# Performance work log

Hardware: AMD Instinct MI355X
Metric: run time of the kernel (lower is better)

Reference implementation:

```python
import jax, jax.numpy as jnp
import numpy as np

N, K, D_IN, D_OUT = 50000, 16, 128, 256
C1, C2 = D_OUT // 4, D_OUT // 2  # 64, 128
E = N * K


def _lin(key, din, dout):
    return jax.random.normal(key, (din, dout), jnp.float32) * 0.02


def setup_inputs() -> dict:
    key = jax.random.key(0)
    ks = jax.random.split(key, 16)
    x = jax.random.normal(ks[0], (N, D_IN), jnp.float32)
    pos = jax.random.normal(ks[1], (N, 3), jnp.float32)
    normals = jax.random.normal(ks[2], (N, 3), jnp.float32)
    batch = jnp.zeros((N,), jnp.int32)
    # fixed k-regular graph standing in for knn_graph(pos, K); src != dst so
    # darboux's sqrt(|pos_j-pos_i|^2) is smooth everywhere
    dst = jnp.repeat(jnp.arange(N, dtype=jnp.int32), K)            # [E]
    off = jax.random.randint(ks[3], (E,), 1, N, jnp.int32)
    src = (dst + off) % N                                          # [E]
    edge_index = jnp.stack([src, dst])                             # [2,E]
    inp = dict(x=x, pos=pos, batch=batch, normals=normals, edge_index=edge_index)

    def add_mlp(name, k, din, dout):
        inp[name + '_w'] = _lin(k, din, dout)
        inp[name + '_b'] = jnp.zeros((dout,), jnp.float32)
        inp[name + '_g'] = jnp.ones((dout,), jnp.float32)
        inp[name + '_bt'] = jnp.zeros((dout,), jnp.float32)

    add_mlp('mlp1', ks[4], D_IN, D_OUT // 8)
    add_mlp('sc', ks[5], D_IN, D_OUT)
    add_mlp('mlp2', ks[6], C2, D_OUT)
    add_mlp('enc1', ks[7], 8, C1 // 2)
    inp['att1_w'] = _lin(ks[8], C1, C1)
    add_mlp('post1', ks[9], C1, C1)
    add_mlp('enc2', ks[10], 8, C2 // 2)
    inp['att2_w'] = _lin(ks[11], C2, C2)
    add_mlp('post2', ks[12], C2, C2)
    return inp


def _bn(h, g, bt, eps=1e-6):
    # BatchNorm1d, training-mode batch statistics (biased variance)
    m = h.mean(0)
    v = jnp.mean((h - m) ** 2, axis=0)
    return (h - m) * jax.lax.rsqrt(v + eps) * g + bt


def _lrelu(h):
    return jnp.where(h >= 0, h, 0.2 * h)


def _smlp(h, w, b, g, bt, act=True):
    # SharedMLP layer: Linear -> BN(eps=1e-6) -> LeakyReLU(0.2) (act optional)
    h = _bn(h @ w + b, g, bt)
    return _lrelu(h) if act else h


def _darboux(pi, pj, ni, nj):
    eps = 1e-10
    d = pj - pi                                            # [E,3]
    dot = lambda a, b: jnp.sum(a * b, axis=1, keepdims=True)
    nrm = lambda a: jnp.sqrt(jnp.sum(a * a, axis=1, keepdims=True))
    dist = nrm(d)
    lni, lnj = nrm(ni), nrm(nj)
    uq = jnp.cross(d, ni); vq = jnp.cross(uq, ni)
    uk = jnp.cross(d, nj); vk = jnp.cross(uk, nj)
    luq, lvq, luk, lvk = nrm(uq), nrm(vq), nrm(uk), nrm(vk)
    return jnp.concatenate([
        dist,
        dot(d, ni) / (dist * lni + eps),
        dot(d, nj) / (dist * lnj + eps),
        dot(ni, nj) / (lni * lnj + eps),
        dot(uq, uk) / (luq * luk + eps),
        dot(vq, vk) / (lvq * lvk + eps),
        dot(uq, vk) / (luq * lvk + eps),
        dot(vq, uk) / (lvq * luk + eps),
    ], axis=1)                                             # [E,8]


def _seg_softmax(h, idx, n):
    m = jax.ops.segment_max(h, idx, num_segments=n)        # [N,C]
    e = jnp.exp(h - m[idx])
    s = jax.ops.segment_sum(e, idx, num_segments=n)
    return e / (s[idx] + 1e-16)


def _lfa(src, dst, n, x, pos, normals, ew, eb, eg, ebt, aw, pw, pb, pg, pbt):
    rel = _darboux(pos[dst], pos[src], normals[dst], normals[src])  # [E,8]
    lse = _smlp(rel, ew, eb, eg, ebt)                               # [E,C/2]
    lf = jnp.concatenate([x[src], lse], axis=1)                     # [E,C]
    att = lf @ aw                                                   # [E,C]
    scores = _seg_softmax(att, dst, n)
    agg = jax.ops.segment_sum(scores * lf, dst, num_segments=n)     # [N,C]
    return _smlp(agg, pw, pb, pg, pbt)


def reference(x, pos, batch, normals, edge_index,
              mlp1_w, mlp1_b, mlp1_g, mlp1_bt,
              sc_w, sc_b, sc_g, sc_bt,
              mlp2_w, mlp2_b, mlp2_g, mlp2_bt,
              enc1_w, enc1_b, enc1_g, enc1_bt, att1_w,
              post1_w, post1_b, post1_g, post1_bt,
              enc2_w, enc2_b, enc2_g, enc2_bt, att2_w,
              post2_w, post2_b, post2_g, post2_bt):
    n = x.shape[0]
    src, dst = edge_index[0], edge_index[1]
    shortcut = _smlp(x, sc_w, sc_b, sc_g, sc_bt, act=False)         # [N,d_out]
    h = _smlp(x, mlp1_w, mlp1_b, mlp1_g, mlp1_bt)                   # [N,d_out//8]
    h = _lfa(src, dst, n, h, pos, normals,
             enc1_w, enc1_b, enc1_g, enc1_bt, att1_w,
             post1_w, post1_b, post1_g, post1_bt)                   # [N,d_out//4]
    h = _lfa(src, dst, n, h, pos, normals,
             enc2_w, enc2_b, enc2_g, enc2_bt, att2_w,
             post2_w, post2_b, post2_g, post2_bt)                   # [N,d_out//2]
    h = _smlp(h, mlp2_w, mlp2_b, mlp2_g, mlp2_bt, act=False)        # [N,d_out]
    return _lrelu(h + shortcut)
```

## Files before the change

### kernel.cpp

```cpp
#include <hip/hip_runtime.h>
#include <hip/hip_bf16.h>
#include <math.h>


typedef __attribute__((ext_vector_type(8))) short short8;
typedef __attribute__((ext_vector_type(4))) float floatx4;

#define NPART 16
#define PSTRIDE 4096

__device__ __forceinline__ float lrelu_f(float v) { return v >= 0.f ? v : 0.2f * v; }

__device__ __forceinline__ uint asu(float f) {
    union { float f; uint u; } c; c.f = f; return c.u;
}
__device__ __forceinline__ unsigned short f2bf(float f) {
    union { __hip_bfloat16 h; unsigned short u; } cv;
    cv.h = __float2bfloat16(f);
    return cv.u;
}
__device__ __forceinline__ unsigned short f2bf_r(float f) {
    return (unsigned short)((asu(f) + 0x8000u) >> 16);
}
__device__ __forceinline__ uint pack2bf_r(float lo, float hi) {
    return ((asu(lo) + 0x8000u) >> 16) | ((asu(hi) + 0x8000u) & 0xFFFF0000u);
}
__device__ __forceinline__ float bf2f(unsigned short u) {
    union { unsigned short u; __hip_bfloat16 h; } cv;
    cv.u = u;
    return __bfloat162float(cv.h);
}

struct PrepSeg { const float* src; short* dst; int cnt; int Cout; int KK; };
struct PrepArgs { PrepSeg seg[6]; };

__global__ void wprep_kernel(PrepArgs pa)
{
    int gid = blockIdx.x * 256 + threadIdx.x;
    int base = 0;
    for (int s = 0; s < 6; s++) {
        int c = pa.seg[s].cnt;
        if (gid < base + c) {
            int fi = gid - base;
            const float* w = pa.seg[s].src;
            const int Cout = pa.seg[s].Cout, KK = pa.seg[s].KK;
            const int l15 = fi & 15, g = (fi >> 4) & 3, rest = fi >> 6;
            const int kk = rest % KK, nt = rest / KK;
            const int col = nt * 16 + l15;
            short8 v;
#pragma unroll
            for (int e = 0; e < 8; e++)
                v[e] = (short)f2bf(w[(size_t)(kk * 32 + g * 8 + e) * Cout + col]);
            *reinterpret_cast<short8*>(pa.seg[s].dst + (size_t)fi * 8) = v;
            return;
        }
        base += c;
    }
}

template<int DIN, int DOUT, int TM>
__global__ void lin_stats_kernel(const float* __restrict__ in, const float* __restrict__ w,
                                 const float* __restrict__ b, float* __restrict__ out,
                                 double* __restrict__ st, int n)
{
    constexpr int CT = DOUT;
    constexpr int RG = 256 / CT;
    constexpr int ROWS = TM * RG;
    __shared__ float xtile[ROWS][DIN];
    double* stp = st + (blockIdx.x & (NPART - 1)) * PSTRIDE;
    const int row0 = blockIdx.x * ROWS;
    for (int idx = threadIdx.x; idx < ROWS * DIN; idx += 256) {
        int r = idx / DIN, j = idx - r * DIN;
        int rr = row0 + r;
        xtile[r][j] = (rr < n) ? in[(size_t)rr * DIN + j] : 0.f;
    }
    __syncthreads();
    const int c  = threadIdx.x % CT;
    const int rg = threadIdx.x / CT;
    float acc[TM];
    const float bv = b[c];
#pragma unroll
    for (int t = 0; t < TM; t++) acc[t] = bv;
    for (int j = 0; j < DIN; j++) {
        float wv = w[(size_t)j * DOUT + c];
#pragma unroll
        for (int t = 0; t < TM; t++) acc[t] = fmaf(xtile[rg * TM + t][j], wv, acc[t]);
    }
    float s = 0.f, s2 = 0.f;
#pragma unroll
    for (int t = 0; t < TM; t++) {
        int rr = row0 + rg * TM + t;
        if (rr < n) {
            out[(size_t)rr * DOUT + c] = acc[t];
            s += acc[t];
            s2 = fmaf(acc[t], acc[t], s2);
        }
    }
    __syncthreads();
    float* ls  = &xtile[0][0];
    float* ls2 = ls + 256;
    ls[threadIdx.x] = s; ls2[threadIdx.x] = s2;
    __syncthreads();
    if (rg == 0) {
#pragma unroll
        for (int g = 1; g < RG; g++) { s += ls[g * CT + c]; s2 += ls2[g * CT + c]; }
        atomicAdd(&stp[c], (double)s);
        atomicAdd(&stp[DOUT + c], (double)s2);
    }
}

template<bool AFF, bool IN16>
__global__ __launch_bounds__(256)
void lin_mfma_kernel(const void* __restrict__ inv, const float* __restrict__ aff,
                     const short* __restrict__ wp, const float* __restrict__ b,
                     unsigned short* __restrict__ out16, double* __restrict__ st, int n)
{
    __shared__ __align__(16) char aS[64 * 256];
    const int tid = threadIdx.x;
    const int w = tid >> 6, grp = (tid >> 4) & 3, l15 = tid & 15, lane = tid & 63;
    const int row0 = blockIdx.x * 64;
    double* stp = st + (blockIdx.x & (NPART - 1)) * PSTRIDE;
    {
        const int r = tid >> 2;
        const int p = tid & 3;
        const int chbase = p * 32;
        const int gr = row0 + r;
        if (gr < n) {
#pragma unroll
            for (int u = 0; u < 4; u++) {
                float h[8];
                if constexpr (IN16) {
                    const unsigned short* hrow = (const unsigned short*)inv + (size_t)gr * 128 + chbase + u * 8;
                    uint4 raw = *reinterpret_cast<const uint4*>(hrow);
                    h[0] = bf2f((unsigned short)(raw.x & 0xFFFF)); h[1] = bf2f((unsigned short)(raw.x >> 16));
                    h[2] = bf2f((unsigned short)(raw.y & 0xFFFF)); h[3] = bf2f((unsigned short)(raw.y >> 16));
                    h[4] = bf2f((unsigned short)(raw.z & 0xFFFF)); h[5] = bf2f((unsigned short)(raw.z >> 16));
                    h[6] = bf2f((unsigned short)(raw.w & 0xFFFF)); h[7] = bf2f((unsigned short)(raw.w >> 16));
                } else {
                    const float* hrow = (const float*)inv + (size_t)gr * 128 + chbase + u * 8;
                    float4 h0 = *reinterpret_cast<const float4*>(hrow);
                    float4 h1 = *reinterpret_cast<const float4*>(hrow + 4);
                    h[0] = h0.x; h[1] = h0.y; h[2] = h0.z; h[3] = h0.w;
                    h[4] = h1.x; h[5] = h1.y; h[6] = h1.z; h[7] = h1.w;
                }
                if constexpr (AFF) {
                    const float* ar = aff + chbase + u * 8;
                    const float* cr = aff + 128 + chbase + u * 8;
#pragma unroll
                    for (int i2 = 0; i2 < 8; i2++)
                        h[i2] = lrelu_f(fmaf(h[i2], ar[i2], cr[i2]));
                }
                uint4 pk;
                pk.x = pack2bf_r(h[0], h[1]); pk.y = pack2bf_r(h[2], h[3]);
                pk.z = pack2bf_r(h[4], h[5]); pk.w = pack2bf_r(h[6], h[7]);
                const int unit = (chbase >> 3) + u;
                *reinterpret_cast<uint4*>(aS + r * 256 + ((unit ^ (r & 7)) << 4)) = pk;
            }
        }
    }
    __syncthreads();

    short8 B[4][4]; float bias[4];
#pragma unroll
    for (int t = 0; t < 4; t++) {
        const int nt = w * 4 + t;
        bias[t] = b[nt * 16 + l15];
#pragma unroll
        for (int kk = 0; kk < 4; kk++)
            B[t][kk] = *reinterpret_cast<const short8*>(wp + (size_t)(((nt * 4 + kk) * 4 + grp) * 16 + l15) * 8);
    }
    float ssum[4] = {0.f, 0.f, 0.f, 0.f}, ssq[4] = {0.f, 0.f, 0.f, 0.f};
#pragma unroll
    for (int mt = 0; mt < 4; mt++) {
        short8 a[4];
        const int arow = mt * 16 + l15;
#pragma unroll
        for (int kk = 0; kk < 4; kk++)
            a[kk] = *reinterpret_cast<const short8*>(aS + arow * 256 + ((((kk << 2) + grp) ^ (arow & 7)) << 4));
#pragma unroll
        for (int t = 0; t < 4; t++) {
            floatx4 acc = {bias[t], bias[t], bias[t], bias[t]};
#pragma unroll
            for (int kk = 0; kk < 4; kk++)
                acc = __builtin_amdgcn_mfma_f32_16x16x32_bf16(a[kk], B[t][kk], acc, 0, 0, 0);
            const int c = (w * 4 + t) * 16 + l15;
#pragma unroll
            for (int r = 0; r < 4; r++) {
                const int grow = row0 + mt * 16 + grp * 4 + r;
                if (grow < n) {
                    out16[(size_t)grow * 256 + c] = f2bf_r(acc[r]);
                    ssum[t] += acc[r];
                    ssq[t] = fmaf(acc[r], acc[r], ssq[t]);
                }
            }
        }
    }
#pragma unroll
    for (int t = 0; t < 4; t++) {
        float s = ssum[t], q = ssq[t];
        s += __shfl_xor(s, 16); s += __shfl_xor(s, 32);
        q += __shfl_xor(q, 16); q += __shfl_xor(q, 32);
        if (lane < 16) {
            const int c = (w * 4 + t) * 16 + l15;
            atomicAdd(&stp[c], (double)s);
            atomicAdd(&stp[256 + c], (double)q);
        }
    }
}

__global__ __launch_bounds__(256)
void edge_enc_kernel(const int* __restrict__ src, const float* __restrict__ pos,
                     const float* __restrict__ nrm, unsigned short* __restrict__ rel16,
                     int E, double* __restrict__ stM)
{
    float s8[8] = {0, 0, 0, 0, 0, 0, 0, 0};
    float M[36];
#pragma unroll
    for (int k = 0; k < 36; k++) M[k] = 0.f;
    const int tid = threadIdx.x;

    for (int e = blockIdx.x * 256 + tid; e < E; e += gridDim.x * 256) {
        const int d = e >> 4;
        const int s = src[e];
        const float pix = pos[3 * d], piy = pos[3 * d + 1], piz = pos[3 * d + 2];
        const float pjx = pos[3 * s], pjy = pos[3 * s + 1], pjz = pos[3 * s + 2];
        const float nix = nrm[3 * d], niy = nrm[3 * d + 1], niz = nrm[3 * d + 2];
        const float njx = nrm[3 * s], njy = nrm[3 * s + 1], njz = nrm[3 * s + 2];
        const float dx = pjx - pix, dy = pjy - piy, dz = pjz - piz;
        const float dist = sqrtf(dx * dx + dy * dy + dz * dz);
        const float lni = sqrtf(nix * nix + niy * niy + niz * niz);
        const float lnj = sqrtf(njx * njx + njy * njy + njz * njz);
        const float uqx = dy * niz - dz * niy, uqy = dz * nix - dx * niz, uqz = dx * niy - dy * nix;
        const float vqx = uqy * niz - uqz * niy, vqy = uqz * nix - uqx * niz, vqz = uqx * niy - uqy * nix;
        const float ukx = dy * njz - dz * njy, uky = dz * njx - dx * njz, ukz = dx * njy - dy * njx;
        const float vkx = uky * njz - ukz * njy, vky = ukz * njx - ukx * njz, vkz = ukx * njy - uky * njx;
        const float luq = sqrtf(uqx * uqx + uqy * uqy + uqz * uqz);
        const float lvq = sqrtf(vqx * vqx + vqy * vqy + vqz * vqz);
        const float luk = sqrtf(ukx * ukx + uky * uky + ukz * ukz);
        const float lvk = sqrtf(vkx * vkx + vky * vky + vkz * vkz);
        const float eps = 1e-10f;
        float rv[8];
        rv[0] = dist;
        rv[1] = (dx * nix + dy * niy + dz * niz) / (dist * lni + eps);
        rv[2] = (dx * njx + dy * njy + dz * njz) / (dist * lnj + eps);
        rv[3] = (nix * njx + niy * njy + niz * njz) / (lni * lnj + eps);
        rv[4] = (uqx * ukx + uqy * uky + uqz * ukz) / (luq * luk + eps);
        rv[5] = (vqx * vkx + vqy * vky + vqz * vkz) / (lvq * lvk + eps);
        rv[6] = (uqx * vkx + uqy * vky + uqz * vkz) / (luq * lvk + eps);
        rv[7] = (vqx * ukx + vqy * uky + vqz * ukz) / (lvq * luk + eps);
        uint4 pk;
        pk.x = pack2bf_r(rv[0], rv[1]); pk.y = pack2bf_r(rv[2], rv[3]);
        pk.z = pack2bf_r(rv[4], rv[5]); pk.w = pack2bf_r(rv[6], rv[7]);
        *reinterpret_cast<uint4*>(rel16 + (size_t)e * 8) = pk;
#pragma unroll
        for (int i = 0; i < 8; i++) s8[i] += rv[i];
#pragma unroll
        for (int i = 0; i < 8; i++)
#pragma unroll
            for (int j = i; j < 8; j++)
                M[i * 8 - (i * (i - 1)) / 2 + (j - i)] = fmaf(rv[i], rv[j], M[i * 8 - (i * (i - 1)) / 2 + (j - i)]);
    }
#pragma unroll
    for (int k = 0; k < 8; k++) {
        float v = s8[k];
        v += __shfl_xor(v, 1); v += __shfl_xor(v, 2); v += __shfl_xor(v, 4);
        v += __shfl_xor(v, 8); v += __shfl_xor(v, 16); v += __shfl_xor(v, 32);
        s8[k] = v;
    }
#pragma unroll
    for (int k = 0; k < 36; k++) {
        float v = M[k];
        v += __shfl_xor(v, 1); v += __shfl_xor(v, 2); v += __shfl_xor(v, 4);
        v += __shfl_xor(v, 8); v += __shfl_xor(v, 16); v += __shfl_xor(v, 32);
        M[k] = v;
    }
    __shared__ float red[4][44];
    const int w = tid >> 6, lane = tid & 63;
    if (lane == 0) {
#pragma unroll
        for (int k = 0; k < 8; k++) red[w][k] = s8[k];
#pragma unroll
        for (int k = 0; k < 36; k++) red[w][8 + k] = M[k];
    }
    __syncthreads();
    if (tid < 44) {
        float tot = red[0][tid] + red[1][tid] + red[2][tid] + red[3][tid];
        atomicAdd(&stM[(blockIdx.x & (NPART - 1)) * PSTRIDE + tid], (double)tot);
    }
}

__global__ void enc_finalize_kernel(const double* __restrict__ stM,
    const float* __restrict__ ew1, const float* __restrict__ eb1,
    const float* __restrict__ g1, const float* __restrict__ bt1, float* __restrict__ ac1,
    const float* __restrict__ ew2, const float* __restrict__ eb2,
    const float* __restrict__ g2, const float* __restrict__ bt2, float* __restrict__ ac2,
    float Ef)
{
    __shared__ double SM[44];
    const int tid = threadIdx.x;
    if (tid < 44) {
        double a = 0;
        for (int p = 0; p < NPART; p++) a += stM[p * PSTRIDE + tid];
        SM[tid] = a;
    }
    __syncthreads();
    if (tid < 96) {
        const bool is2 = tid < 64;
        const int c = is2 ? tid : tid - 64;
        const int HCc = is2 ? 64 : 32;
        const float* ew = is2 ? ew2 : ew1;
        const float b = (is2 ? eb2 : eb1)[c];
        float wv[8];
#pragma unroll
        for (int j = 0; j < 8; j++) wv[j] = ew[j * HCc + c];
        double dot = 0.0, quad = 0.0;
#pragma unroll
        for (int i = 0; i < 8; i++) {
            dot += SM[i] * (double)wv[i];
#pragma unroll
            for (int j = i; j < 8; j++) {
                const double mij = SM[8 + i * 8 - (i * (i - 1)) / 2 + (j - i)];
                quad += mij * (double)wv[i] * (double)wv[j] * ((i == j) ? 1.0 : 2.0);
            }
        }
        const double sum   = dot + (double)Ef * b;
        const double sumsq = quad + 2.0 * b * dot + (double)Ef * b * b;
        const double m = sum / Ef;
        const double v = sumsq / Ef - m * m;
        const float rstd = (float)(1.0 / sqrt(v + 1e-6));
        const float a = rstd * (is2 ? g2 : g1)[c];
        float* ac = is2 ? ac2 : ac1;
        ac[c] = a;
        ac[HCc + c] = fmaf(-(float)m, a, (is2 ? bt2 : bt1)[c]);
    }
}

struct FinSeg { const double* st; const float* g; const float* bt; float* ac; int C; float cnt; };
struct FinArgs { FinSeg seg[3]; };

__global__ void finalize_multi_kernel(FinArgs fa)
{
    FinSeg s = fa.seg[blockIdx.x];
    int c = threadIdx.x;
    if (c < s.C) {
        double sm = 0.0, sq = 0.0;
#pragma unroll
        for (int p = 0; p < NPART; p++) {
            sm += s.st[p * PSTRIDE + c];
            sq += s.st[p * PSTRIDE + s.C + c];
        }
        double m = sm / (double)s.cnt;
        double v = sq / (double)s.cnt - m * m;
        float rstd = (float)(1.0 / sqrt(v + 1e-6));
        float a = rstd * s.g[c];
        s.ac[c] = a;
        s.ac[s.C + c] = fmaf(-(float)m, a, s.bt[c]);
    }
}

template<int C, bool IN16>
__global__ void bnconv_kernel(const void* __restrict__ hv, const float* __restrict__ ac,
                              unsigned short* __restrict__ o, size_t total8)
{
    size_t i = (size_t)blockIdx.x * blockDim.x + threadIdx.x;
    size_t stride = (size_t)gridDim.x * blockDim.x;
    for (; i < total8; i += stride) {
        const size_t b = i * 8;
        const int c = (int)(b & (size_t)(C - 1));
        float h[8];
        if constexpr (IN16) {
            uint4 raw = *reinterpret_cast<const uint4*>((const unsigned short*)hv + b);
            h[0] = bf2f((unsigned short)(raw.x & 0xFFFF)); h[1] = bf2f((unsigned short)(raw.x >> 16));
            h[2] = bf2f((unsigned short)(raw.y & 0xFFFF)); h[3] = bf2f((unsigned short)(raw.y >> 16));
            h[4] = bf2f((unsigned short)(raw.z & 0xFFFF)); h[5] = bf2f((unsigned short)(raw.z >> 16));
            h[6] = bf2f((unsigned short)(raw.w & 0xFFFF)); h[7] = bf2f((unsigned short)(raw.w >> 16));
        } else {
            float4 h0 = *reinterpret_cast<const float4*>((const float*)hv + b);
            float4 h1 = *reinterpret_cast<const float4*>((const float*)hv + b + 4);
            h[0] = h0.x; h[1] = h0.y; h[2] = h0.z; h[3] = h0.w;
            h[4] = h1.x; h[5] = h1.y; h[6] = h1.z; h[7] = h1.w;
        }
        const float* ar = ac + c;
        const float* cr = ac + C + c;
        uint4 pk;
        pk.x = pack2bf_r(lrelu_f(fmaf(h[0], ar[0], cr[0])), lrelu_f(fmaf(h[1], ar[1], cr[1])));
        pk.y = pack2bf_r(lrelu_f(fmaf(h[2], ar[2], cr[2])), lrelu_f(fmaf(h[3], ar[3], cr[3])));
        pk.z = pack2bf_r(lrelu_f(fmaf(h[4], ar[4], cr[4])), lrelu_f(fmaf(h[5], ar[5], cr[5])));
        pk.w = pack2bf_r(lrelu_f(fmaf(h[6], ar[6], cr[6])), lrelu_f(fmaf(h[7], ar[7], cr[7])));
        *reinterpret_cast<uint4*>(o + b) = pk;
    }
}

template<int C, int NODES>
__global__ __launch_bounds__(256)
void lfa11_kernel(const unsigned short* __restrict__ hbn,
                  const unsigned short* __restrict__ rel16,
                  const int* __restrict__ src,
                  const float* __restrict__ ew, const float* __restrict__ eb,
                  const float* __restrict__ encac,
                  const short* __restrict__ attp, const short* __restrict__ postp,
                  const float* __restrict__ postb,
                  unsigned short* __restrict__ out16, double* __restrict__ st, int n)
{
    constexpr int HC = C / 2, NT = C / 16, NTW = NT / 4, KK = C / 32, ROWB = 2 * C;
    constexpr int ROWS = NODES * 16;
    constexpr int TPR = 256 / ROWS;
    constexpr int NTE = HC / 16;
    constexpr int NCOMB = (NODES * NTE) / 4;
    constexpr int NSTEP = 4 / NTE;

    __shared__ __align__(16) char lfS[ROWS * ROWB];
    __shared__ __align__(16) char aggS[16 * ROWB];

    const int tid = threadIdx.x;
    const int lane = tid & 63, w = tid >> 6, grp = (tid >> 4) & 3, l15 = tid & 15;
    const int node0 = blockIdx.x * NODES;
    const int e0g = node0 * 16;
    const int Etot = n * 16;
    const int kk_sel = (w * NTW) >> 1;
    double* stp = st + (blockIdx.x & (NPART - 1)) * PSTRIDE;

    if constexpr (NODES < 16) {
        for (int i = tid; i < (16 - NODES) * ROWB / 16; i += 256)
            reinterpret_cast<uint4*>(aggS + NODES * ROWB)[i] = (uint4){0, 0, 0, 0};
    }

    short8 Batt[NTW][KK], Bsel[NTW];
#pragma unroll
    for (int t = 0; t < NTW; t++) {
        const int nt = w * NTW + t;
#pragma unroll
        for (int kk = 0; kk < KK; kk++)
            Batt[t][kk] = *reinterpret_cast<const short8*>(attp + (size_t)(((nt * KK + kk) * 4 + grp) * 16 + l15) * 8);
        const int ng = ((nt & 1) << 1) | (l15 >> 3);
#pragma unroll
        for (int e = 0; e < 8; e++)
            Bsel[t][e] = (grp == ng && (l15 & 7) == e) ? (short)0x3F80 : (short)0;
    }

    const int etile = w % NTE;
    const int cc = etile * 16 + l15;
    short8 Benc = {0, 0, 0, 0, 0, 0, 0, 0};
    if (grp == 0) {
#pragma unroll
        for (int j = 0; j < 8; j++) Benc[j] = (short)f2bf(ew[j * HC + cc]);
    }
    const float encA = encac[cc];
    const float encB2 = fmaf(encA, eb[cc], encac[HC + cc]);
    const int cfull = HC + cc;
    const int cuE = cfull >> 3, subE = (cfull & 7) * 2;

    {
        const int r = (TPR == 1) ? tid : (tid / TPR);
        const int p = (TPR == 1) ? 0 : (tid % TPR);
        constexpr int CHT = HC / TPR;
        const int chb = p * CHT;
        const int eg = e0g + r;
        if (eg < Etot) {
            const int s = src[eg];
            const unsigned short* hrow = hbn + (size_t)s * HC + chb;
#pragma unroll
            for (int u = 0; u < CHT / 8; u++) {
                uint4 pk = *reinterpret_cast<const uint4*>(hrow + u * 8);
                const int unit = (chb >> 3) + u;
                *reinterpret_cast<uint4*>(lfS + r * ROWB + ((unit ^ (r & 7)) << 4)) = pk;
            }
        }
    }

    {
        const int nodeStart = w / NTE;
#pragma unroll
        for (int j = 0; j < NCOMB; j++) {
            const int node = nodeStart + j * NSTEP;
            const int r0 = node * 16;
            int eg = e0g + r0 + l15;
            if (eg >= Etot) eg = Etot - 1;
            const short8 Arel = *reinterpret_cast<const short8*>(rel16 + (size_t)eg * 8);
            floatx4 accE = {0.f, 0.f, 0.f, 0.f};
            accE = __builtin_amdgcn_mfma_f32_16x16x32_bf16(Arel, Benc, accE, 0, 0, 0);
#pragma unroll
            for (int r = 0; r < 4; r++) {
                const int row = r0 + grp * 4 + r;
                const float tv = lrelu_f(fmaf(accE[r], encA, encB2));
                *reinterpret_cast<unsigned short*>(lfS + row * ROWB + ((cuE ^ (row & 7)) << 4) + subE) = f2bf_r(tv);
            }
        }
    }
    __syncthreads();

    for (int mt = 0; mt < NODES; ++mt) {
        const int arow = mt * 16 + l15;
        const char* rbase = lfS + arow * ROWB;
        const int x7 = l15 & 7;
        short8 a[KK];
#pragma unroll
        for (int kk = 0; kk < KK; kk++)
            a[kk] = *reinterpret_cast<const short8*>(rbase + ((((kk << 2) + grp) ^ x7) << 4));
        const short8 asel = *reinterpret_cast<const short8*>(rbase + ((((kk_sel << 2) + grp) ^ x7) << 4));
        floatx4 acc[NTW], Lc[NTW];
#pragma unroll
        for (int t = 0; t < NTW; t++) {
            acc[t] = (floatx4){0.f, 0.f, 0.f, 0.f};
            Lc[t] = (floatx4){0.f, 0.f, 0.f, 0.f};
        }
#pragma unroll
        for (int t = 0; t < NTW; t++)
            Lc[t] = __builtin_amdgcn_mfma_f32_16x16x32_bf16(asel, Bsel[t], Lc[t], 0, 0, 0);
#pragma unroll
        for (int kk = 0; kk < KK; kk++)
#pragma unroll
            for (int t = 0; t < NTW; t++)
                acc[t] = __builtin_amdgcn_mfma_f32_16x16x32_bf16(a[kk], Batt[t][kk], acc[t], 0, 0, 0);

#pragma unroll
        for (int t = 0; t < NTW; t++) {
            float e0 = __expf(acc[t][0]), e1 = __expf(acc[t][1]);
            float e2 = __expf(acc[t][2]), e3 = __expf(acc[t][3]);
            float ss = (e0 + e1) + (e2 + e3);
            ss += __shfl_xor(ss, 16);
            ss += __shfl_xor(ss, 32);
            const float inv = 1.f / (ss + 1e-16f);
            float av = fmaf(e0, Lc[t][0], fmaf(e1, Lc[t][1], fmaf(e2, Lc[t][2], e3 * Lc[t][3])));
            av += __shfl_xor(av, 16);
            av += __shfl_xor(av, 32);
            av *= inv;
            if (lane < 16) {
                const int c = (w * NTW + t) * 16 + l15;
                const int cu = c >> 3, sub = (c & 7) * 2;
                *reinterpret_cast<unsigned short*>(aggS + mt * ROWB + ((cu ^ (mt & 7)) << 4) + sub) = f2bf_r(av);
            }
        }
    }
    __syncthreads();

    short8 Bpost[NTW][KK]; float pb[NTW];
#pragma unroll
    for (int t = 0; t < NTW; t++) {
        const int nt = w * NTW + t;
        pb[t] = postb[nt * 16 + l15];
#pragma unroll
        for (int kk = 0; kk < KK; kk++)
            Bpost[t][kk] = *reinterpret_cast<const short8*>(postp + (size_t)(((nt * KK + kk) * 4 + grp) * 16 + l15) * 8);
    }
    short8 ag[KK];
#pragma unroll
    for (int kk = 0; kk < KK; kk++)
        ag[kk] = *reinterpret_cast<const short8*>(aggS + l15 * ROWB + ((((kk << 2) + grp) ^ (l15 & 7)) << 4));
    floatx4 accP[NTW];
#pragma unroll
    for (int t = 0; t < NTW; t++) accP[t] = (floatx4){0.f, 0.f, 0.f, 0.f};
#pragma unroll
    for (int kk = 0; kk < KK; kk++)
#pragma unroll
        for (int t = 0; t < NTW; t++)
            accP[t] = __builtin_amdgcn_mfma_f32_16x16x32_bf16(ag[kk], Bpost[t][kk], accP[t], 0, 0, 0);
#pragma unroll
    for (int t = 0; t < NTW; t++) {
        const int c = (w * NTW + t) * 16 + l15;
        float s = 0.f, q = 0.f;
#pragma unroll
        for (int r = 0; r < 4; r++) {
            const int nb = grp * 4 + r;
            if (nb < NODES && node0 + nb < n) {
                const float v = accP[t][r] + pb[t];
                out16[(size_t)(node0 + nb) * C + c] = f2bf_r(v);
                s += v;
                q = fmaf(v, v, q);
            }
        }
        s += __shfl_xor(s, 16); s += __shfl_xor(s, 32);
        q += __shfl_xor(q, 16); q += __shfl_xor(q, 32);
        if (lane < 16) {
            atomicAdd(&stp[c], (double)s);
            atomicAdd(&stp[C + c], (double)q);
        }
    }
}

__global__ void final_kernel(float* __restrict__ out, const unsigned short* __restrict__ m2,
                             const unsigned short* __restrict__ xs,
                             const float* __restrict__ ac2, const float* __restrict__ acs,
                             int total4)
{
    int i = blockIdx.x * 256 + threadIdx.x;
    const int stride = gridDim.x * 256;
    for (; i < total4; i += stride) {
        ushort4 mv = reinterpret_cast<const ushort4*>(m2)[i];
        ushort4 xv = reinterpret_cast<const ushort4*>(xs)[i];
        const int c = (i & 63) << 2;
        float4 a2 = *reinterpret_cast<const float4*>(ac2 + c);
        float4 b2 = *reinterpret_cast<const float4*>(ac2 + 256 + c);
        float4 as = *reinterpret_cast<const float4*>(acs + c);
        float4 bs = *reinterpret_cast<const float4*>(acs + 256 + c);
        float4 v;
        v.x = lrelu_f(fmaf(bf2f(mv.x), a2.x, b2.x) + fmaf(bf2f(xv.x), as.x, bs.x));
        v.y = lrelu_f(fmaf(bf2f(mv.y), a2.y, b2.y) + fmaf(bf2f(xv.y), as.y, bs.y));
        v.z = lrelu_f(fmaf(bf2f(mv.z), a2.z, b2.z) + fmaf(bf2f(xv.z), as.z, bs.z));
        v.w = lrelu_f(fmaf(bf2f(mv.w), a2.w, b2.w) + fmaf(bf2f(xv.w), as.w, bs.w));
        reinterpret_cast<float4*>(out)[i] = v;
    }
}

extern "C" void kernel_launch(void* const* d_in, const int* in_sizes, int n_in,
                              void* d_out, int out_size, void* d_ws, size_t ws_size,
                              hipStream_t stream)
{
    const float* x       = (const float*)d_in[0];
    const float* pos     = (const float*)d_in[1];
    const float* normals = (const float*)d_in[3];
    const int*   eidx    = (const int*)d_in[4];

    const float* mlp1_w = (const float*)d_in[5];
    const float* mlp1_b = (const float*)d_in[6];
    const float* mlp1_g = (const float*)d_in[7];
    const float* mlp1_bt= (const float*)d_in[8];
    const float* sc_w   = (const float*)d_in[9];
    const float* sc_b   = (const float*)d_in[10];
    const float* sc_g   = (const float*)d_in[11];
    const float* sc_bt  = (const float*)d_in[12];
    const float* mlp2_w = (const float*)d_in[13];
    const float* mlp2_b = (const float*)d_in[14];
    const float* mlp2_g = (const float*)d_in[15];
    const float* mlp2_bt= (const float*)d_in[16];
    const float* enc1_w = (const float*)d_in[17];
    const float* enc1_b = (const float*)d_in[18];
    const float* enc1_g = (const float*)d_in[19];
    const float* enc1_bt= (const float*)d_in[20];
    const float* att1_w = (const float*)d_in[21];
    const float* post1_w = (const float*)d_in[22];
    const float* post1_b = (const float*)d_in[23];
    const float* post1_g = (const float*)d_in[24];
    const float* post1_bt= (const float*)d_in[25];
    const float* enc2_w = (const float*)d_in[26];
    const float* enc2_b = (const float*)d_in[27];
    const float* enc2_g = (const float*)d_in[28];
    const float* enc2_bt= (const float*)d_in[29];
    const float* att2_w = (const float*)d_in[30];
    const float* post2_w = (const float*)d_in[31];
    const float* post2_b = (const float*)d_in[32];
    const float* post2_g = (const float*)d_in[33];
    const float* post2_bt= (const float*)d_in[34];

    float* out = (float*)d_out;

    const int n = in_sizes[0] / 128;
    const int E = in_sizes[4] / 2;
    const int* srcArr = eidx;

    char* base = (char*)d_ws;
    double* stats  = (double*)base;
    float*  affine = (float*)(base + 524288);
    short*  wprep  = (short*)(base + 540672);
    unsigned short* rel16 = (unsigned short*)(base + 786432);
    unsigned short* xs16  = rel16 + (size_t)E * 8;
    unsigned short* m2pre = xs16 + (size_t)n * 256;
    float*  h1   = (float*)(m2pre + (size_t)n * 256);
    unsigned short* hA16 = (unsigned short*)(h1 + (size_t)n * 32);
    unsigned short* hB16 = hA16 + (size_t)n * 64;
    unsigned short* h1bn = hB16;
    unsigned short* hAbn = (unsigned short*)h1;

    short* att1p = wprep;
    short* post1p = wprep + 4096;
    short* att2p = wprep + 8192;
    short* post2p = wprep + 24576;
    short* scp   = wprep + 40960;
    short* mlp2p = wprep + 73728;

    const int OF_MLP1 = 0, OF_ENCM = 64, OF_POST1 = 128, OF_POST2 = 512, OF_SC = 768, OF_MLP2 = 1280;
    const int AF_MLP1 = 0, AF_ENC1 = 64, AF_POST1 = 128, AF_ENC2 = 256,
              AF_POST2 = 512, AF_SC = 768, AF_MLP2 = 1280;

    hipMemsetAsync(stats, 0, NPART * 32768, stream);

    PrepArgs pa;
    pa.seg[0] = {att1_w,  att1p,  512,  64,  2};
    pa.seg[1] = {post1_w, post1p, 512,  64,  2};
    pa.seg[2] = {att2_w,  att2p,  2048, 128, 4};
    pa.seg[3] = {post2_w, post2p, 2048, 128, 4};
    pa.seg[4] = {sc_w,    scp,    4096, 256, 4};
    pa.seg[5] = {mlp2_w,  mlp2p,  4096, 256, 4};
    wprep_kernel<<<52, 256, 0, stream>>>(pa);

    lin_stats_kernel<128, 32, 8><<<(n + 63) / 64, 256, 0, stream>>>(x, mlp1_w, mlp1_b, h1, stats + OF_MLP1, n);
    lin_mfma_kernel<false, false><<<(n + 63) / 64, 256, 0, stream>>>(x, nullptr, scp, sc_b, xs16, stats + OF_SC, n);

    edge_enc_kernel<<<512, 256, 0, stream>>>(srcArr, pos, normals, rel16, E, stats + OF_ENCM);

    FinArgs f1;
    f1.seg[0] = {stats + OF_MLP1, mlp1_g, mlp1_bt, affine + AF_MLP1, 32, (float)n};
    f1.seg[1] = f1.seg[0]; f1.seg[2] = f1.seg[0];
    finalize_multi_kernel<<<1, 256, 0, stream>>>(f1);
    enc_finalize_kernel<<<1, 128, 0, stream>>>(stats + OF_ENCM,
        enc1_w, enc1_b, enc1_g, enc1_bt, affine + AF_ENC1,
        enc2_w, enc2_b, enc2_g, enc2_bt, affine + AF_ENC2, (float)E);

    bnconv_kernel<32, false><<<1024, 256, 0, stream>>>(h1, affine + AF_MLP1, h1bn, (size_t)n * 32 / 8);

    lfa11_kernel<64, 16><<<(n + 15) / 16, 256, 0, stream>>>(h1bn, rel16, srcArr, enc1_w, enc1_b,
        affine + AF_ENC1, att1p, post1p, post1_b, hA16, stats + OF_POST1, n);
    FinArgs f2;
    f2.seg[0] = {stats + OF_POST1, post1_g, post1_bt, affine + AF_POST1, 64, (float)n};
    f2.seg[1] = f2.seg[0]; f2.seg[2] = f2.seg[0];
    finalize_multi_kernel<<<1, 256, 0, stream>>>(f2);

    bnconv_kernel<64, true><<<1024, 256, 0, stream>>>(hA16, affine + AF_POST1, hAbn, (size_t)n * 64 / 8);

    lfa11_kernel<128, 8><<<(n + 7) / 8, 256, 0, stream>>>(hAbn, rel16, srcArr, enc2_w, enc2_b,
        affine + AF_ENC2, att2p, post2p, post2_b, hB16, stats + OF_POST2, n);
    FinArgs f3;
    f3.seg[0] = {stats + OF_POST2, post2_g, post2_bt, affine + AF_POST2, 128, (float)n};
    f3.seg[1] = f3.seg[0]; f3.seg[2] = f3.seg[0];
    finalize_multi_kernel<<<1, 256, 0, stream>>>(f3);

    lin_mfma_kernel<true, true><<<(n + 63) / 64, 256, 0, stream>>>(hB16, affine + AF_POST2, mlp2p, mlp2_b,
        m2pre, stats + OF_MLP2, n);
    FinArgs f4;
    f4.seg[0] = {stats + OF_MLP2, mlp2_g, mlp2_bt, affine + AF_MLP2, 256, (float)n};
    f4.seg[1] = {stats + OF_SC,   sc_g,   sc_bt,   affine + AF_SC,   256, (float)n};
    f4.seg[2] = f4.seg[0];
    finalize_multi_kernel<<<2, 256, 0, stream>>>(f4);

    final_kernel<<<2048, 256, 0, stream>>>(out, m2pre, xs16, affine + AF_MLP2, affine + AF_SC, n * 64);
}
```

Before: 258.3 us.

## Fuse mlp1 linear into shortcut MFMA kernel and process two node tiles per iteration

```diff
diff --git a/kernel.cpp b/kernel.cpp
--- a/kernel.cpp
+++ b/kernel.cpp
@@ -32,13 +32,13 @@
 }
 
 struct PrepSeg { const float* src; short* dst; int cnt; int Cout; int KK; };
-struct PrepArgs { PrepSeg seg[6]; };
+struct PrepArgs { PrepSeg seg[7]; };
 
 __global__ void wprep_kernel(PrepArgs pa)
 {
     int gid = blockIdx.x * 256 + threadIdx.x;
     int base = 0;
-    for (int s = 0; s < 6; s++) {
+    for (int s = 0; s < 7; s++) {
         int c = pa.seg[s].cnt;
         if (gid < base + c) {
             int fi = gid - base;
@@ -58,68 +58,20 @@
     }
 }
 
-template<int DIN, int DOUT, int TM>
-__global__ void lin_stats_kernel(const float* __restrict__ in, const float* __restrict__ w,
-                                 const float* __restrict__ b, float* __restrict__ out,
-                                 double* __restrict__ st, int n)
-{
-    constexpr int CT = DOUT;
-    constexpr int RG = 256 / CT;
-    constexpr int ROWS = TM * RG;
-    __shared__ float xtile[ROWS][DIN];
-    double* stp = st + (blockIdx.x & (NPART - 1)) * PSTRIDE;
-    const int row0 = blockIdx.x * ROWS;
-    for (int idx = threadIdx.x; idx < ROWS * DIN; idx += 256) {
-        int r = idx / DIN, j = idx - r * DIN;
-        int rr = row0 + r;
-        xtile[r][j] = (rr < n) ? in[(size_t)rr * DIN + j] : 0.f;
-    }
-    __syncthreads();
-    const int c  = threadIdx.x % CT;
-    const int rg = threadIdx.x / CT;
-    float acc[TM];
-    const float bv = b[c];
-#pragma unroll
-    for (int t = 0; t < TM; t++) acc[t] = bv;
-    for (int j = 0; j < DIN; j++) {
-        float wv = w[(size_t)j * DOUT + c];
-#pragma unroll
-        for (int t = 0; t < TM; t++) acc[t] = fmaf(xtile[rg * TM + t][j], wv, acc[t]);
-    }
-    float s = 0.f, s2 = 0.f;
-#pragma unroll
-    for (int t = 0; t < TM; t++) {
-        int rr = row0 + rg * TM + t;
-        if (rr < n) {
-            out[(size_t)rr * DOUT + c] = acc[t];
-            s += acc[t];
-            s2 = fmaf(acc[t], acc[t], s2);
-        }
-    }
-    __syncthreads();
-    float* ls  = &xtile[0][0];
-    float* ls2 = ls + 256;
-    ls[threadIdx.x] = s; ls2[threadIdx.x] = s2;
-    __syncthreads();
-    if (rg == 0) {
-#pragma unroll
-        for (int g = 1; g < RG; g++) { s += ls[g * CT + c]; s2 += ls2[g * CT + c]; }
-        atomicAdd(&stp[c], (double)s);
-        atomicAdd(&stp[DOUT + c], (double)s2);
-    }
-}
-
-template<bool AFF, bool IN16>
+template<bool AFF, bool IN16, bool MLP1>
 __global__ __launch_bounds__(256)
 void lin_mfma_kernel(const void* __restrict__ inv, const float* __restrict__ aff,
                      const short* __restrict__ wp, const float* __restrict__ b,
-                     unsigned short* __restrict__ out16, double* __restrict__ st, int n)
+                     unsigned short* __restrict__ out16, double* __restrict__ st,
+                     const short* __restrict__ wp1, const float* __restrict__ b1,
+                     unsigned short* __restrict__ out1, double* __restrict__ st1, int n)
 {
     __shared__ __align__(16) char aS[64 * 256];
     const int tid = threadIdx.x;
     const int w = tid >> 6, grp = (tid >> 4) & 3, l15 = tid & 15, lane = tid & 63;
     const int row0 = blockIdx.x * 64;
-    double* stp = st + (blockIdx.x & (NPART - 1)) * PSTRIDE;
+    const int poff = (blockIdx.x & (NPART - 1)) * PSTRIDE;
+    double* stp = st + poff;
     {
         const int r = tid >> 2;
         const int p = tid & 3;
@@ -204,6 +156,47 @@
             const int c = (w * 4 + t) * 16 + l15;
             atomicAdd(&stp[c], (double)s);
             atomicAdd(&stp[256 + c], (double)q);
+        }
+    }
+
+    if constexpr (MLP1) {
+        if (w < 2) {
+            double* stp1 = st1 + poff;
+            const float bias1 = b1[w * 16 + l15];
+            short8 B1[4];
+#pragma unroll
+            for (int kk = 0; kk < 4; kk++)
+                B1[kk] = *reinterpret_cast<const short8*>(wp1 + (size_t)(((w * 4 + kk) * 4 + grp) * 16 + l15) * 8);
+            float s1 = 0.f, q1 = 0.f;
+#pragma unroll
+            for (int mt = 0; mt < 4; mt++) {
+                short8 a[4];
+                const int arow = mt * 16 + l15;
+#pragma unroll
+                for (int kk = 0; kk < 4; kk++)
+                    a[kk] = *reinterpret_cast<const short8*>(aS + arow * 256 + ((((kk << 2) + grp) ^ (arow & 7)) << 4));
+                floatx4 acc = {bias1, bias1, bias1, bias1};
+#pragma unroll
+                for (int kk = 0; kk < 4; kk++)
+                    acc = __builtin_amdgcn_mfma_f32_16x16x32_bf16(a[kk], B1[kk], acc, 0, 0, 0);
+                const int c = w * 16 + l15;
+#pragma unroll
+                for (int r = 0; r < 4; r++) {
+                    const int grow = row0 + mt * 16 + grp * 4 + r;
+                    if (grow < n) {
+                        out1[(size_t)grow * 32 + c] = f2bf_r(acc[r]);
+                        s1 += acc[r];
+                        q1 = fmaf(acc[r], acc[r], q1);
+                    }
+                }
+            }
+            s1 += __shfl_xor(s1, 16); s1 += __shfl_xor(s1, 32);
+            q1 += __shfl_xor(q1, 16); q1 += __shfl_xor(q1, 32);
+            if (lane < 16) {
+                const int c = w * 16 + l15;
+                atomicAdd(&stp1[c], (double)s1);
+                atomicAdd(&stp1[32 + c], (double)q1);
+            }
         }
     }
 }
@@ -358,8 +351,8 @@
     }
 }
 
-template<int C, bool IN16>
-__global__ void bnconv_kernel(const void* __restrict__ hv, const float* __restrict__ ac,
+template<int C>
+__global__ void bnconv_kernel(const unsigned short* __restrict__ hv, const float* __restrict__ ac,
                               unsigned short* __restrict__ o, size_t total8)
 {
     size_t i = (size_t)blockIdx.x * blockDim.x + threadIdx.x;
@@ -367,19 +360,12 @@
     for (; i < total8; i += stride) {
         const size_t b = i * 8;
         const int c = (int)(b & (size_t)(C - 1));
+        uint4 raw = *reinterpret_cast<const uint4*>(hv + b);
         float h[8];
-        if constexpr (IN16) {
-            uint4 raw = *reinterpret_cast<const uint4*>((const unsigned short*)hv + b);
-            h[0] = bf2f((unsigned short)(raw.x & 0xFFFF)); h[1] = bf2f((unsigned short)(raw.x >> 16));
-            h[2] = bf2f((unsigned short)(raw.y & 0xFFFF)); h[3] = bf2f((unsigned short)(raw.y >> 16));
-            h[4] = bf2f((unsigned short)(raw.z & 0xFFFF)); h[5] = bf2f((unsigned short)(raw.z >> 16));
-            h[6] = bf2f((unsigned short)(raw.w & 0xFFFF)); h[7] = bf2f((unsigned short)(raw.w >> 16));
-        } else {
-            float4 h0 = *reinterpret_cast<const float4*>((const float*)hv + b);
-            float4 h1 = *reinterpret_cast<const float4*>((const float*)hv + b + 4);
-            h[0] = h0.x; h[1] = h0.y; h[2] = h0.z; h[3] = h0.w;
-            h[4] = h1.x; h[5] = h1.y; h[6] = h1.z; h[7] = h1.w;
-        }
+        h[0] = bf2f((unsigned short)(raw.x & 0xFFFF)); h[1] = bf2f((unsigned short)(raw.x >> 16));
+        h[2] = bf2f((unsigned short)(raw.y & 0xFFFF)); h[3] = bf2f((unsigned short)(raw.y >> 16));
+        h[4] = bf2f((unsigned short)(raw.z & 0xFFFF)); h[5] = bf2f((unsigned short)(raw.z >> 16));
+        h[6] = bf2f((unsigned short)(raw.w & 0xFFFF)); h[7] = bf2f((unsigned short)(raw.w >> 16));
         const float* ar = ac + c;
         const float* cr = ac + C + c;
         uint4 pk;
@@ -393,7 +379,7 @@
 
 template<int C, int NODES>
 __global__ __launch_bounds__(256)
-void lfa11_kernel(const unsigned short* __restrict__ hbn,
+void lfa12_kernel(const unsigned short* __restrict__ hbn,
                   const unsigned short* __restrict__ rel16,
                   const int* __restrict__ src,
                   const float* __restrict__ ew, const float* __restrict__ eb,
@@ -489,46 +475,68 @@
     }
     __syncthreads();
 
-    for (int mt = 0; mt < NODES; ++mt) {
-        const int arow = mt * 16 + l15;
-        const char* rbase = lfS + arow * ROWB;
+    for (int mt0 = 0; mt0 < NODES; mt0 += 2) {
         const int x7 = l15 & 7;
-        short8 a[KK];
+        const int arowA = mt0 * 16 + l15;
+        const int arowB = arowA + 16;
+        const char* rbA = lfS + arowA * ROWB;
+        const char* rbB = lfS + arowB * ROWB;
+        short8 aA[KK], aB[KK];
+#pragma unroll
+        for (int kk = 0; kk < KK; kk++) {
+            aA[kk] = *reinterpret_cast<const short8*>(rbA + ((((kk << 2) + grp) ^ x7) << 4));
+            aB[kk] = *reinterpret_cast<const short8*>(rbB + ((((kk << 2) + grp) ^ x7) << 4));
+        }
+        const short8 aselA = *reinterpret_cast<const short8*>(rbA + ((((kk_sel << 2) + grp) ^ x7) << 4));
+        const short8 aselB = *reinterpret_cast<const short8*>(rbB + ((((kk_sel << 2) + grp) ^ x7) << 4));
+        floatx4 accA[NTW], accB[NTW], LcA[NTW], LcB[NTW];
+#pragma unroll
+        for (int t = 0; t < NTW; t++) {
+            accA[t] = (floatx4){0.f, 0.f, 0.f, 0.f};
+            accB[t] = (floatx4){0.f, 0.f, 0.f, 0.f};
+            LcA[t] = (floatx4){0.f, 0.f, 0.f, 0.f};
+            LcB[t] = (floatx4){0.f, 0.f, 0.f, 0.f};
+        }
+#pragma unroll
+        for (int t = 0; t < NTW; t++) {
+            LcA[t] = __builtin_amdgcn_mfma_f32_16x16x32_bf16(aselA, Bsel[t], LcA[t], 0, 0, 0);
+            LcB[t] = __builtin_amdgcn_mfma_f32_16x16x32_bf16(aselB, Bsel[t], LcB[t], 0, 0, 0);
+        }
 #pragma unroll
         for (int kk = 0; kk < KK; kk++)
-            a[kk] = *reinterpret_cast<const short8*>(rbase + ((((kk << 2) + grp) ^ x7) << 4));
-        const short8 asel = *reinterpret_cast<const short8*>(rbase + ((((kk_sel << 2) + grp) ^ x7) << 4));
-        floatx4 acc[NTW], Lc[NTW];
+#pragma unroll
+            for (int t = 0; t < NTW; t++) {
+                accA[t] = __builtin_amdgcn_mfma_f32_16x16x32_bf16(aA[kk], Batt[t][kk], accA[t], 0, 0, 0);
+                accB[t] = __builtin_amdgcn_mfma_f32_16x16x32_bf16(aB[kk], Batt[t][kk], accB[t], 0, 0, 0);
+            }
+
 #pragma unroll
         for (int t = 0; t < NTW; t++) {
-            acc[t] = (floatx4){0.f, 0.f, 0.f, 0.f};
-            Lc[t] = (floatx4){0.f, 0.f, 0.f, 0.f};
-        }
-#pragma unroll
-        for (int t = 0; t < NTW; t++)
-            Lc[t] = __builtin_amdgcn_mfma_f32_16x16x32_bf16(asel, Bsel[t], Lc[t], 0, 0, 0);
-#pragma unroll
-        for (int kk = 0; kk < KK; kk++)
-#pragma unroll
-            for (int t = 0; t < NTW; t++)
-                acc[t] = __builtin_amdgcn_mfma_f32_16x16x32_bf16(a[kk], Batt[t][kk], acc[t], 0, 0, 0);
-
-#pragma unroll
-        for (int t = 0; t < NTW; t++) {
-            float e0 = __expf(acc[t][0]), e1 = __expf(acc[t][1]);
-            float e2 = __expf(acc[t][2]), e3 = __expf(acc[t][3]);
-            float ss = (e0 + e1) + (e2 + e3);
-            ss += __shfl_xor(ss, 16);
-            ss += __shfl_xor(ss, 32);
-            const float inv = 1.f / (ss + 1e-16f);
-            float av = fmaf(e0, Lc[t][0], fmaf(e1, Lc[t][1], fmaf(e2, Lc[t][2], e3 * Lc[t][3])));
-            av += __shfl_xor(av, 16);
-            av += __shfl_xor(av, 32);
-            av *= inv;
+            float e0A = __expf(accA[t][0]), e1A = __expf(accA[t][1]);
+            float e2A = __expf(accA[t][2]), e3A = __expf(accA[t][3]);
+            float e0B = __expf(accB[t][0]), e1B = __expf(accB[t][1]);
+            float e2B = __expf(accB[t][2]), e3B = __expf(accB[t][3]);
+            float ssA = (e0A + e1A) + (e2A + e3A);
+            float ssB = (e0B + e1B) + (e2B + e3B);
+            ssA += __shfl_xor(ssA, 16);
+            ssB += __shfl_xor(ssB, 16);
+            ssA += __shfl_xor(ssA, 32);
+            ssB += __shfl_xor(ssB, 32);
+            const float invA = 1.f / (ssA + 1e-16f);
+            const float invB = 1.f / (ssB + 1e-16f);
+            float avA = fmaf(e0A, LcA[t][0], fmaf(e1A, LcA[t][1], fmaf(e2A, LcA[t][2], e3A * LcA[t][3])));
+            float avB = fmaf(e0B, LcB[t][0], fmaf(e1B, LcB[t][1], fmaf(e2B, LcB[t][2], e3B * LcB[t][3])));
+            avA += __shfl_xor(avA, 16);
+            avB += __shfl_xor(avB, 16);
+            avA += __shfl_xor(avA, 32);
+            avB += __shfl_xor(avB, 32);
+            avA *= invA;
+            avB *= invB;
             if (lane < 16) {
                 const int c = (w * NTW + t) * 16 + l15;
                 const int cu = c >> 3, sub = (c & 7) * 2;
-                *reinterpret_cast<unsigned short*>(aggS + mt * ROWB + ((cu ^ (mt & 7)) << 4) + sub) = f2bf_r(av);
+                *reinterpret_cast<unsigned short*>(aggS + mt0 * ROWB + ((cu ^ (mt0 & 7)) << 4) + sub) = f2bf_r(avA);
+                *reinterpret_cast<unsigned short*>(aggS + (mt0 + 1) * ROWB + ((cu ^ ((mt0 + 1) & 7)) << 4) + sub) = f2bf_r(avB);
             }
         }
     }
@@ -655,11 +663,11 @@
     unsigned short* rel16 = (unsigned short*)(base + 786432);
     unsigned short* xs16  = rel16 + (size_t)E * 8;
     unsigned short* m2pre = xs16 + (size_t)n * 256;
-    float*  h1   = (float*)(m2pre + (size_t)n * 256);
-    unsigned short* hA16 = (unsigned short*)(h1 + (size_t)n * 32);
-    unsigned short* hB16 = hA16 + (size_t)n * 64;
-    unsigned short* h1bn = hB16;
-    unsigned short* hAbn = (unsigned short*)h1;
+    unsigned short* h1raw = m2pre + (size_t)n * 256;
+    unsigned short* h1bn  = h1raw + (size_t)n * 32;
+    unsigned short* hA16  = h1bn + (size_t)n * 32;
+    unsigned short* hAbn  = hA16 + (size_t)n * 64;
+    unsigned short* hB16  = hAbn + (size_t)n * 64;
 
     short* att1p = wprep;
     short* post1p = wprep + 4096;
@@ -667,6 +675,7 @@
     short* post2p = wprep + 24576;
     short* scp   = wprep + 40960;
     short* mlp2p = wprep + 73728;
+    short* mlp1p = wprep + 106496;
 
     const int OF_MLP1 = 0, OF_ENCM = 64, OF_POST1 = 128, OF_POST2 = 512, OF_SC = 768, OF_MLP2 = 1280;
     const int AF_MLP1 = 0, AF_ENC1 = 64, AF_POST1 = 128, AF_ENC2 = 256,
@@ -681,10 +690,12 @@
     pa.seg[3] = {post2_w, post2p, 2048, 128, 4};
     pa.seg[4] = {sc_w,    scp,    4096, 256, 4};
     pa.seg[5] = {mlp2_w,  mlp2p,  4096, 256, 4};
-    wprep_kernel<<<52, 256, 0, stream>>>(pa);
-
-    lin_stats_kernel<128, 32, 8><<<(n + 63) / 64, 256, 0, stream>>>(x, mlp1_w, mlp1_b, h1, stats + OF_MLP1, n);
-    lin_mfma_kernel<false, false><<<(n + 63) / 64, 256, 0, stream>>>(x, nullptr, scp, sc_b, xs16, stats + OF_SC, n);
+    pa.seg[6] = {mlp1_w,  mlp1p,  512,  32,  4};
+    wprep_kernel<<<54, 256, 0, stream>>>(pa);
+
+    lin_mfma_kernel<false, false, true><<<(n + 63) / 64, 256, 0, stream>>>(
+        x, nullptr, scp, sc_b, xs16, stats + OF_SC,
+        mlp1p, mlp1_b, h1raw, stats + OF_MLP1, n);
 
     edge_enc_kernel<<<512, 256, 0, stream>>>(srcArr, pos, normals, rel16, E, stats + OF_ENCM);
 
@@ -696,26 +707,27 @@
         enc1_w, enc1_b, enc1_g, enc1_bt, affine + AF_ENC1,
         enc2_w, enc2_b, enc2_g, enc2_bt, affine + AF_ENC2, (float)E);
 
-    bnconv_kernel<32, false><<<1024, 256, 0, stream>>>(h1, affine + AF_MLP1, h1bn, (size_t)n * 32 / 8);
-
-    lfa11_kernel<64, 16><<<(n + 15) / 16, 256, 0, stream>>>(h1bn, rel16, srcArr, enc1_w, enc1_b,
+    bnconv_kernel<32><<<1024, 256, 0, stream>>>(h1raw, affine + AF_MLP1, h1bn, (size_t)n * 32 / 8);
+
+    lfa12_kernel<64, 16><<<(n + 15) / 16, 256, 0, stream>>>(h1bn, rel16, srcArr, enc1_w, enc1_b,
         affine + AF_ENC1, att1p, post1p, post1_b, hA16, stats + OF_POST1, n);
     FinArgs f2;
     f2.seg[0] = {stats + OF_POST1, post1_g, post1_bt, affine + AF_POST1, 64, (float)n};
     f2.seg[1] = f2.seg[0]; f2.seg[2] = f2.seg[0];
     finalize_multi_kernel<<<1, 256, 0, stream>>>(f2);
 
-    bnconv_kernel<64, true><<<1024, 256, 0, stream>>>(hA16, affine + AF_POST1, hAbn, (size_t)n * 64 / 8);
-
-    lfa11_kernel<128, 8><<<(n + 7) / 8, 256, 0, stream>>>(hAbn, rel16, srcArr, enc2_w, enc2_b,
+    bnconv_kernel<64><<<1024, 256, 0, stream>>>(hA16, affine + AF_POST1, hAbn, (size_t)n * 64 / 8);
+
+    lfa12_kernel<128, 8><<<(n + 7) / 8, 256, 0, stream>>>(hAbn, rel16, srcArr, enc2_w, enc2_b,
         affine + AF_ENC2, att2p, post2p, post2_b, hB16, stats + OF_POST2, n);
     FinArgs f3;
     f3.seg[0] = {stats + OF_POST2, post2_g, post2_bt, affine + AF_POST2, 128, (float)n};
     f3.seg[1] = f3.seg[0]; f3.seg[2] = f3.seg[0];
     finalize_multi_kernel<<<1, 256, 0, stream>>>(f3);
 
-    lin_mfma_kernel<true, true><<<(n + 63) / 64, 256, 0, stream>>>(hB16, affine + AF_POST2, mlp2p, mlp2_b,
-        m2pre, stats + OF_MLP2, n);
+    lin_mfma_kernel<true, true, false><<<(n + 63) / 64, 256, 0, stream>>>(
+        hB16, affine + AF_POST2, mlp2p, mlp2_b, m2pre, stats + OF_MLP2,
+        nullptr, nullptr, nullptr, nullptr, n);
     FinArgs f4;
     f4.seg[0] = {stats + OF_MLP2, mlp2_g, mlp2_bt, affine + AF_MLP2, 256, (float)n};
     f4.seg[1] = {stats + OF_SC,   sc_g,   sc_bt,   affine + AF_SC,   256, (float)n};
```

New measurement: 239.7 us. -7.2%, faster.
